# Kernel optimization log

Measured on AMD Instinct MI355X. Metric: run time of the kernel, lower is better.

## Reference

```python
import jax, jax.numpy as jnp
import numpy as np

B, T, F, H, O = 256, 1024, 128, 512, 64
BN_EPS = 1e-5


def setup_inputs() -> dict:
    key = jax.random.key(0)
    ks = jax.random.split(key, 24)
    p = lambda k, shape: 0.02 * jax.random.normal(k, shape, dtype=jnp.float32)
    inp = {
        "x": jax.random.normal(ks[0], (B, T, F), dtype=jnp.float32),
        "delta": jax.random.uniform(ks[1], (B, T, F), dtype=jnp.float32),
        "m": (jax.random.uniform(ks[2], (B, T, F)) > 0.5).astype(jnp.float32),
        "x_forward": jax.random.normal(ks[3], (B, T, F), dtype=jnp.float32),
        # packed-sequence style: descending number of active rows per timestep
        "batch_sizes": jnp.sort(jax.random.randint(ks[4], (T,), 1, B + 1))[::-1].astype(jnp.int32),
        "W_r": p(ks[5], (F, H)), "U_r": p(ks[6], (H, H)), "V_r": p(ks[7], (F, H)), "b_r": jnp.zeros((H,), jnp.float32),
        "W_z": p(ks[8], (F, H)), "U_z": p(ks[9], (H, H)), "V_z": p(ks[10], (F, H)), "b_z": jnp.zeros((H,), jnp.float32),
        "W": p(ks[11], (F, H)), "U": p(ks[12], (H, H)), "V": p(ks[13], (F, H)), "b": jnp.zeros((H,), jnp.float32),
        "W_gamma_x": p(ks[14], (F,)), "b_gamma_x": jnp.zeros((F,), jnp.float32),
        "W_gamma_h": p(ks[15], (F, H)), "b_gamma_h": jnp.zeros((H,), jnp.float32),
        "dec_W": p(ks[16], (H, O)), "dec_b": jnp.zeros((O,), jnp.float32),
        "bn_w": jnp.ones((H,), jnp.float32), "bn_b": jnp.zeros((H,), jnp.float32),
    }
    return inp


def reference(x, delta, m, x_forward, batch_sizes,
              W_r, U_r, V_r, b_r, W_z, U_z, V_z, b_z, W, U, V, b,
              W_gamma_x, b_gamma_x, W_gamma_h, b_gamma_h,
              dec_W, dec_b, bn_w, bn_b):
    # input decay gamma_x: [B,T,F]; hidden decay gamma_h: [B,T,H]
    gamma_x = jnp.exp(-jax.nn.relu(delta * W_gamma_x + b_gamma_x))
    gamma_h = jnp.exp(-jax.nn.relu(jnp.einsum("btf,fh->bth", m, W_gamma_h) + b_gamma_h))
    # impute observed (m==1) positions with decayed forward-fill (matches x[m.byte()] = x_replace[m.byte()])
    x_rep = gamma_x * x_forward + (1.0 - gamma_x) * 0.001
    x = jnp.where(m > 0.5, x_rep, x)

    # time-major for scan
    xT = jnp.transpose(x, (1, 0, 2))        # [T,B,F]
    mT = jnp.transpose(m, (1, 0, 2))        # [T,B,F]
    gT = jnp.transpose(gamma_h, (1, 0, 2))  # [T,B,H]
    row = jnp.arange(B)

    def step(h, inp):
        x_t, m_t, g_t, bs = inp
        mask = (row < bs)[:, None]          # active rows this step
        h_d = jnp.where(mask, g_t * h, h)   # decayed hidden (index_copy_ on [:bs])
        one_m = 1.0 - m_t
        z = jax.nn.sigmoid(x_t @ W_z + h_d @ U_z + one_m @ V_z + b_z)
        r = jax.nn.sigmoid(x_t @ W_r + h_d @ U_r + one_m @ V_r + b_r)
        h_tilde = jnp.tanh(x_t @ W + (h_d * r) @ U + one_m @ V + b)
        h_new = jnp.where(mask, (1.0 - z) * h_d + z * h_tilde, h_d)
        return h_new, None

    h0 = jnp.zeros((B, H), jnp.float32)
    h_t, _ = jax.lax.scan(step, h0, (xT, mT, gT, batch_sizes))

    # eval-mode BatchNorm1d (running_mean=0, running_var=1); batch_size>1 so BN applies
    h_bn = h_t * (bn_w / jnp.sqrt(1.0 + BN_EPS)) + bn_b
    output = jax.nn.log_softmax(h_bn @ dec_W + dec_b, axis=-1)
    return output, h_bn
```

## Files before the change

### kernel.cpp

```cpp
#include <hip/hip_runtime.h>
#include <hip/hip_bf16.h>

typedef __attribute__((ext_vector_type(8))) short bf16x8;
typedef __attribute__((ext_vector_type(4))) float f32x4;
typedef __attribute__((ext_vector_type(4))) float fvec4;
typedef __attribute__((ext_vector_type(4))) unsigned short u16x4;
typedef __attribute__((ext_vector_type(4))) int i32x4;

#define DEVI __device__ __forceinline__

constexpr int BB = 256, TT = 1024, FF = 128, HH = 512, OO = 64;
constexpr int KK = 256;
constexpr int NN = 2048;

DEVI unsigned short f2bf(float x) {
  unsigned int u = __float_as_uint(x);
  u += 0x7FFFu + ((u >> 16) & 1u);
  return (unsigned short)(u >> 16);
}
DEVI float bf2f(unsigned short s) {
  return __uint_as_float(((unsigned int)s) << 16);
}

DEVI void gload16(const void* g, void* lds) {
  __builtin_amdgcn_global_load_lds(
      (const __attribute__((address_space(1))) void*)g,
      (__attribute__((address_space(3))) void*)lds, 16, 0, 0);
}

DEVI void barrier_lds() {
  asm volatile("s_waitcnt lgkmcnt(0)" ::: "memory");
  __builtin_amdgcn_s_barrier();
  __builtin_amdgcn_sched_barrier(0);
}

DEVI int hgIdx(int row, int c) { return row*1024 + (c ^ ((row & 7) << 3)); }

__global__ __launch_bounds__(256) void prep_scales_kernel(
    const float* __restrict__ U_z, const float* __restrict__ U_r,
    const float* __restrict__ Uh, float* __restrict__ uscale)
{
  int n = blockIdx.x * 256 + threadIdx.x;
  if (n >= 1536) return;
  const float* src = (n < 512) ? U_z : (n < 1024) ? U_r : Uh;
  int col = n & 511;
  float s = 0.f;
  for (int k = 0; k < HH; ++k) s = fmaxf(s, fabsf(src[k*HH + col]));
  uscale[n] = fmaxf(s, 1e-30f);
}

__global__ __launch_bounds__(256) void prep_kernel(
    const float* __restrict__ W_z, const float* __restrict__ V_z, const float* __restrict__ b_z,
    const float* __restrict__ W_r, const float* __restrict__ V_r, const float* __restrict__ b_r,
    const float* __restrict__ Wh,  const float* __restrict__ Vh,  const float* __restrict__ bh,
    const float* __restrict__ Wgh, const float* __restrict__ bgh,
    const float* __restrict__ U_z, const float* __restrict__ U_r, const float* __restrict__ Uh,
    const float* __restrict__ uscale,
    unsigned short* __restrict__ BwT, float* __restrict__ bias,
    int* __restrict__ UzrQ, int* __restrict__ UhQ)
{
  int idx = blockIdx.x * 256 + threadIdx.x;
  if (idx < 524288) {
    int n = idx >> 8, k = idx & 255;
    float v;
    if (n < 512)       { int h = n;        v = (k < 128) ? W_z[k*HH + h] : -V_z[(k-128)*HH + h]; }
    else if (n < 1024) { int h = n - 512;  v = (k < 128) ? W_r[k*HH + h] : -V_r[(k-128)*HH + h]; }
    else if (n < 1536) { int h = n - 1024; v = (k < 128) ? Wh [k*HH + h] : -Vh [(k-128)*HH + h]; }
    else               { int h = n - 1536; v = (k < 128) ? 0.f : Wgh[(k-128)*HH + h]; }
    BwT[n*256 + k] = f2bf(v);
    return;
  }
  idx -= 524288;
  if (idx < 2048) {
    int n = idx; float v;
    if (n < 512)       { float s = b_z[n];      for (int f = 0; f < FF; ++f) s += V_z[f*HH + n];        v = s; }
    else if (n < 1024) { int h = n-512;  float s = b_r[h]; for (int f = 0; f < FF; ++f) s += V_r[f*HH + h]; v = s; }
    else if (n < 1536) { int h = n-1024; float s = bh[h];  for (int f = 0; f < FF; ++f) s += Vh[f*HH + h];  v = s; }
    else               { v = bgh[n-1536]; }
    bias[n] = v;
    return;
  }
  idx -= 2048;
  if (idx < 131072) {
    int j0 = (idx & 3) * 4;
    int l  = (idx >> 2) & 63;
    int nt = (idx >> 8) & 63;
    int kt = idx >> 14;
    int col = (nt & 31)*16 + (l & 15);
    const float* src = (nt < 32) ? U_z : U_r;
    float sc = 127.f / uscale[(nt < 32 ? 0 : 512) + col];
    int word = 0;
#pragma unroll
    for (int b = 0; b < 4; ++b) {
      int k = kt*64 + (l >> 4)*16 + j0 + b;
      float q = fminf(fmaxf(rintf(src[k*HH + col] * sc), -127.f), 127.f);
      word |= ((int)q & 0xFF) << (8*b);
    }
    UzrQ[idx] = word;
    return;
  }
  idx -= 131072;
  if (idx < 65536) {
    int j0 = (idx & 3) * 4;
    int l  = (idx >> 2) & 63;
    int nt = (idx >> 8) & 31;
    int kt = idx >> 13;
    int col = nt*16 + (l & 15);
    float sc = 127.f / uscale[1024 + col];
    int word = 0;
#pragma unroll
    for (int b = 0; b < 4; ++b) {
      int k = kt*64 + (l >> 4)*16 + j0 + b;
      float q = fminf(fmaxf(rintf(Uh[k*HH + col] * sc), -127.f), 127.f);
      word |= ((int)q & 0xFF) << (8*b);
    }
    UhQ[idx] = word;
  }
}

__global__ __launch_bounds__(256) void build_A_kernel(
    const float* __restrict__ x, const float* __restrict__ delta,
    const float* __restrict__ mm, const float* __restrict__ xf,
    const float* __restrict__ Wgx, const float* __restrict__ bgx,
    const int* __restrict__ bs, unsigned short* __restrict__ A,
    int t0, int TC)
{
  int blk = blockIdx.x;
  int row8 = blk * 8;
  int b0  = row8 / TC;
  int tl0 = row8 % TC;
  if (b0 >= bs[t0 + tl0]) return;
  int tid = threadIdx.x;
  int rl = row8 + (tid >> 5);
  int tc = tl0 + (tid >> 5);
  long gi = ((long)b0*TT + t0 + tc) * 32 + (tid & 31);
  int f0 = (tid & 31) * 4;
  fvec4 xv = ((const fvec4*)x)[gi];
  fvec4 dv = ((const fvec4*)delta)[gi];
  fvec4 mv = ((const fvec4*)mm)[gi];
  fvec4 fv = ((const fvec4*)xf)[gi];
  unsigned short ox[4], om[4];
#pragma unroll
  for (int j = 0; j < 4; ++j) {
    float g  = __expf(-fmaxf(dv[j]*Wgx[f0+j] + bgx[f0+j], 0.f));
    float xr = g*fv[j] + (1.f - g)*0.001f;
    float xi = (mv[j] > 0.5f) ? xr : xv[j];
    ox[j] = f2bf(xi); om[j] = f2bf(mv[j]);
  }
  *(u16x4*)(A + (long)rl*KK + f0)       = (u16x4){ox[0], ox[1], ox[2], ox[3]};
  *(u16x4*)(A + (long)rl*KK + 128 + f0) = (u16x4){om[0], om[1], om[2], om[3]};
}

__global__ __launch_bounds__(256) void gemm1_kernel(
    const unsigned short* __restrict__ A, const unsigned short* __restrict__ BwT,
    const float* __restrict__ bias, const int* __restrict__ bs,
    unsigned short* __restrict__ PRE, int t0, int TC)
{
  int blk = blockIdx.x;
  int nt = blk & 15;
  int mt = blk >> 4;
  {
    int m0 = mt * 128;
    int b_ = m0 / TC;
    int bcheck = (TC >= 128) ? bs[t0 + (m0 % TC)] : bs[t0];
    if (b_ >= bcheck) return;
  }
  int tid = threadIdx.x;
  int w = tid >> 6, l = tid & 63;
  int wm = w >> 1, wn = w & 1;
  int lr = l & 15, lg = l >> 4;
  int m_base = mt*128 + wm*64;
  int n_base = nt*128 + wn*64;
  const unsigned short* Aptr = A   + (long)(m_base + lr)*KK + lg*8;
  const unsigned short* Bptr = BwT + (long)(n_base + lr)*KK + lg*8;
  f32x4 acc[4][4];
#pragma unroll
  for (int i = 0; i < 4; ++i)
#pragma unroll
    for (int j = 0; j < 4; ++j) acc[i][j] = (f32x4){0.f, 0.f, 0.f, 0.f};

#pragma unroll
  for (int kt = 0; kt < 8; ++kt) {
    bf16x8 af[4], bfr[4];
#pragma unroll
    for (int i = 0; i < 4; ++i) af[i]  = *(const bf16x8*)(Aptr + (long)i*16*KK + kt*32);
#pragma unroll
    for (int i = 0; i < 4; ++i) bfr[i] = *(const bf16x8*)(Bptr + (long)i*16*KK + kt*32);
#pragma unroll
    for (int ms = 0; ms < 4; ++ms)
#pragma unroll
      for (int ns = 0; ns < 4; ++ns)
        acc[ms][ns] = __builtin_amdgcn_mfma_f32_16x16x32_bf16(af[ms], bfr[ns], acc[ms][ns], 0, 0, 0);
  }
#pragma unroll
  for (int ms = 0; ms < 4; ++ms) {
    int gm0 = m_base + ms*16 + lg*4;
#pragma unroll
    for (int ns = 0; ns < 4; ++ns) {
      int gn = n_base + ns*16 + lr;
      float bv = bias[gn];
      bool is_gamma = (gn >= 1536);
#pragma unroll
      for (int q = 0; q < 4; ++q) {
        float v = acc[ms][ns][q] + bv;
        if (is_gamma) v = __expf(-fmaxf(v, 0.f));
        PRE[(long)(gm0 + q)*NN + gn] = f2bf(v);
      }
    }
  }
}

__global__ __launch_bounds__(512) void scan_kernel(
    const unsigned short* __restrict__ PRE,
    const signed char* __restrict__ UzrQ,
    const signed char* __restrict__ UhQ,
    const float* __restrict__ uscale,
    const int* __restrict__ bs,
    float* __restrict__ h_st,
    float* __restrict__ sbuf,
    int t0, int TC)
{
  __shared__ __align__(16) signed char Ubuf[8][2][4096];
  __shared__ __align__(16) i32x4 hd_l[8*64];
  __shared__ __align__(16) unsigned short slabHG[16*1024];
  __shared__ float hm[16][524];
  __shared__ float wmax[8];

  const int tid = threadIdx.x;
  const int r0 = blockIdx.x * 16;
  if (t0 > 0 && bs[t0] <= r0) return;

  const int w = tid >> 6, l = tid & 63, lr = l & 15, lg = l >> 4;
  const size_t rowStr = (size_t)TC * NN;

  signed char* slot0 = &Ubuf[w][0][0];
  signed char* slot1 = &Ubuf[w][1][0];

  auto STAGEA = [&](int u) {
    const signed char* src = UzrQ + ((size_t)(((u>>1)*64 + (u&1)*32 + w*4)*64) + l)*16;
    signed char* dst = (u & 1) ? slot1 : slot0;
#pragma unroll
    for (int i = 0; i < 4; ++i) gload16(src + (size_t)i*1024, dst + i*1024);
  };
  auto STAGEB = [&](int u) {
    const signed char* src = UhQ + ((size_t)((u*32 + w*4)*64) + l)*16;
    signed char* dst = (u & 1) ? slot1 : slot0;
#pragma unroll
    for (int i = 0; i < 4; ++i) gload16(src + (size_t)i*1024, dst + i*1024);
  };
  auto STAGEHG = [&](const unsigned short* PREn) {
#pragma unroll
    for (int j = 0; j < 4; ++j) {
      int idx = w*4 + j;
      int row = idx >> 1;
      int phys = (idx & 1)*512 + l*8;
      int logi = phys ^ ((row & 7) << 3);
      const unsigned short* src = PREn + (size_t)row*rowStr + 1024 + logi;
      gload16(src, &slabHG[idx*512]);
    }
  };

  float zdq[4], rdq[4], hdq[4];
#pragma unroll
  for (int i = 0; i < 4; ++i) {
    int c = (w*4 + i)*16 + lr;
    zdq[i] = uscale[c]        * (1.f/16129.f);
    rdq[i] = uscale[512 + c]  * (1.f/16129.f);
    hdq[i] = uscale[1024 + c] * (1.f/16129.f);
  }
  if (tid < 8) wmax[tid] = (t0 == 0) ? 1e-20f : sbuf[blockIdx.x];

  if (t0 == 0) {
    for (int i = tid; i < 16*512; i += 512) hm[i>>9][i&511] = 0.f;
  } else {
    for (int i = tid; i < 16*512; i += 512)
      hm[i>>9][i&511] = h_st[(size_t)(r0 + (i>>9))*HH + (i&511)];
  }
  __builtin_amdgcn_sched_barrier(0);

  STAGEHG(PRE + (size_t)r0*TC*NN);
  STAGEA(0); STAGEA(1);

  for (int tc = 0; tc < TC; ++tc) {
    const int bsv = bs[t0 + tc];
    if (bsv <= r0) break;
    const int na = min(16, bsv - r0);
    const unsigned short* PREstep = PRE + ((size_t)r0*TC + tc)*NN;
    const unsigned short* PREnext = PREstep + NN;

    barrier_lds();
    asm volatile("s_waitcnt vmcnt(8)" ::: "memory");
    __builtin_amdgcn_sched_barrier(0);

    float s = wmax[0];
#pragma unroll
    for (int i = 1; i < 8; ++i) s = fmaxf(s, wmax[i]);
    const float qs = 127.f / s;

    unsigned short pzr[2][4][4];
#pragma unroll
    for (int i = 0; i < 4; ++i)
#pragma unroll
      for (int q = 0; q < 4; ++q) {
        int row = lg*4 + q, col = (w*4 + i)*16 + lr;
        const unsigned short* pb = PREstep + (size_t)row*rowStr + col;
        pzr[0][i][q] = pb[0];
        pzr[1][i][q] = pb[512];
      }
    __builtin_amdgcn_sched_barrier(0);

    {
      const int k0 = w*64 + lg*16;
      const bool act = lr < na;
      bf16x8 g0 = *(const bf16x8*)&slabHG[hgIdx(lr, 512 + k0)];
      bf16x8 g1 = *(const bf16x8*)&slabHG[hgIdx(lr, 512 + k0 + 8)];
      i32x4 qw;
#pragma unroll
      for (int d = 0; d < 4; ++d) {
        int word = 0;
#pragma unroll
        for (int b = 0; b < 4; ++b) {
          int j = d*4 + b;
          float h  = hm[lr][k0 + j];
          float gv = bf2f((unsigned short)(j < 8 ? g0[j] : g1[j-8]));
          float hd = act ? gv*h : h;
          float q  = fminf(fmaxf(rintf(hd*qs), -127.f), 127.f);
          word |= ((int)q & 0xFF) << (8*b);
        }
        qw[d] = word;
      }
      hd_l[w*64 + l] = qw;
    }

    float phv[4][4], ggv[4][4];
#pragma unroll
    for (int i = 0; i < 4; ++i)
#pragma unroll
      for (int q = 0; q < 4; ++q) {
        int row = lg*4 + q, col = (w*4 + i)*16 + lr;
        phv[i][q] = bf2f(slabHG[hgIdx(row, col)]);
        ggv[i][q] = bf2f(slabHG[hgIdx(row, 512 + col)]);
      }
    barrier_lds();

    i32x4 acc[8];
#pragma unroll
    for (int i = 0; i < 8; ++i) acc[i] = (i32x4){0, 0, 0, 0};
    i32x4 af;
#pragma unroll
    for (int u = 0; u < 16; ++u) {
      asm volatile("s_waitcnt vmcnt(4)" ::: "memory");
      __builtin_amdgcn_sched_barrier(0);
      const signed char* buf = (u & 1) ? slot1 : slot0;
      if (!(u & 1)) af = hd_l[(u>>1)*64 + l];
#pragma unroll
      for (int i = 0; i < 4; ++i) {
        i32x4 bfr = ((const i32x4*)buf)[i*64 + l];
        acc[(u&1)*4 + i] = __builtin_amdgcn_mfma_i32_16x16x64_i8(af, bfr, acc[(u&1)*4 + i], 0, 0, 0);
      }
      __builtin_amdgcn_sched_barrier(0);
      if (u < 14)       STAGEA(u + 2);
      else if (u == 14) STAGEB(0);
      else              STAGEB(1);
    }

    float zreg[4][4];
#pragma unroll
    for (int i = 0; i < 4; ++i)
#pragma unroll
      for (int q = 0; q < 4; ++q) {
        int row = lg*4 + q, col = (w*4 + i)*16 + lr;
        float az = bf2f(pzr[0][i][q]) + (float)acc[i][q]   * zdq[i] * s;
        float ar = bf2f(pzr[1][i][q]) + (float)acc[4+i][q] * rdq[i] * s;
        zreg[i][q] = 1.f/(1.f + __expf(-az));
        slabHG[hgIdx(row, col)] = f2bf(1.f/(1.f + __expf(-ar)));
      }
    barrier_lds();

    {
      const int k0 = w*64 + lg*16;
      bf16x8 r0v = *(const bf16x8*)&slabHG[hgIdx(lr, k0)];
      bf16x8 r1v = *(const bf16x8*)&slabHG[hgIdx(lr, k0 + 8)];
      i32x4 qw = hd_l[w*64 + l], nw;
#pragma unroll
      for (int d = 0; d < 4; ++d) {
        int word = qw[d], out = 0;
#pragma unroll
        for (int b = 0; b < 4; ++b) {
          int j = d*4 + b;
          int hq = (int)(signed char)((word >> (8*b)) & 0xFF);
          float rv = bf2f((unsigned short)(j < 8 ? r0v[j] : r1v[j-8]));
          float q = fminf(fmaxf(rintf((float)hq * rv), -127.f), 127.f);
          out |= ((int)q & 0xFF) << (8*b);
        }
        nw[d] = out;
      }
      hd_l[w*64 + l] = nw;
    }
    barrier_lds();

    i32x4 accB[4];
#pragma unroll
    for (int i = 0; i < 4; ++i) accB[i] = (i32x4){0, 0, 0, 0};
#pragma unroll
    for (int u = 0; u < 8; ++u) {
      asm volatile("s_waitcnt vmcnt(4)" ::: "memory");
      __builtin_amdgcn_sched_barrier(0);
      const signed char* buf = (u & 1) ? slot1 : slot0;
      i32x4 af2 = hd_l[u*64 + l];
#pragma unroll
      for (int i = 0; i < 4; ++i) {
        i32x4 bfr = ((const i32x4*)buf)[i*64 + l];
        accB[i] = __builtin_amdgcn_mfma_i32_16x16x64_i8(af2, bfr, accB[i], 0, 0, 0);
      }
      __builtin_amdgcn_sched_barrier(0);
      if (u < 6)       STAGEB(u + 2);
      else if (u == 6) STAGEHG(PREnext);
      else             STAGEA(0);
    }
    STAGEA(1);

    float mloc = 0.f;
#pragma unroll
    for (int i = 0; i < 4; ++i)
#pragma unroll
      for (int q = 0; q < 4; ++q) {
        int row = lg*4 + q, col = (w*4 + i)*16 + lr;
        float hval;
        if (row < na) {
          float ah = phv[i][q] + (float)accB[i][q] * hdq[i] * s;
          float e  = __expf(2.f*ah);
          float th = 1.f - 2.f/(e + 1.f);
          float hd = ggv[i][q] * hm[row][col];
          hval = hd + zreg[i][q]*(th - hd);
          hm[row][col] = hval;
        } else {
          hval = hm[row][col];
        }
        mloc = fmaxf(mloc, fabsf(hval));
      }
#pragma unroll
    for (int off = 32; off > 0; off >>= 1) mloc = fmaxf(mloc, __shfl_xor(mloc, off));
    if (l == 0) wmax[w] = fmaxf(mloc, 1e-20f);
  }

  asm volatile("s_waitcnt vmcnt(0)" ::: "memory");
  barrier_lds();
  for (int i = tid; i < 16*512; i += 512)
    h_st[(size_t)(r0 + (i>>9))*HH + (i&511)] = hm[i>>9][i&511];
  if (tid == 0) {
    float s = wmax[0];
#pragma unroll
    for (int i = 1; i < 8; ++i) s = fmaxf(s, wmax[i]);
    sbuf[blockIdx.x] = s;
  }
}

__global__ __launch_bounds__(64) void head_kernel(
    const float* __restrict__ h_state, const float* __restrict__ decW,
    const float* __restrict__ decb, const float* __restrict__ bnw,
    const float* __restrict__ bnb, float* __restrict__ out)
{
  int b = blockIdx.x, o = threadIdx.x;
  __shared__ float hbn[HH];
  const float s = rsqrtf(1.f + 1e-5f);
  for (int j = o; j < HH; j += 64)
    hbn[j] = h_state[(long)b*HH + j] * (bnw[j] * s) + bnb[j];
  __syncthreads();
  float acc = decb[o];
  for (int j = 0; j < HH; ++j) acc += hbn[j] * decW[j*OO + o];
  float mx = acc;
#pragma unroll
  for (int off = 32; off > 0; off >>= 1) mx = fmaxf(mx, __shfl_xor(mx, off));
  float ex = __expf(acc - mx);
  float sum = ex;
#pragma unroll
  for (int off = 32; off > 0; off >>= 1) sum += __shfl_xor(sum, off);
  out[(long)b*OO + o] = acc - mx - __logf(sum);
  for (int j = o; j < HH; j += 64)
    out[(long)BB*OO + (long)b*HH + j] = hbn[j];
}

extern "C" void kernel_launch(void* const* d_in, const int* in_sizes, int n_in,
                              void* d_out, int out_size, void* d_ws, size_t ws_size,
                              hipStream_t stream) {
  const float* x     = (const float*)d_in[0];
  const float* delta = (const float*)d_in[1];
  const float* mm    = (const float*)d_in[2];
  const float* xf    = (const float*)d_in[3];
  const int*   bs    = (const int*)  d_in[4];
  const float* W_r   = (const float*)d_in[5];
  const float* U_r   = (const float*)d_in[6];
  const float* V_r   = (const float*)d_in[7];
  const float* b_r   = (const float*)d_in[8];
  const float* W_z   = (const float*)d_in[9];
  const float* U_z   = (const float*)d_in[10];
  const float* V_z   = (const float*)d_in[11];
  const float* b_z   = (const float*)d_in[12];
  const float* W     = (const float*)d_in[13];
  const float* U     = (const float*)d_in[14];
  const float* V     = (const float*)d_in[15];
  const float* b     = (const float*)d_in[16];
  const float* Wgx   = (const float*)d_in[17];
  const float* bgx   = (const float*)d_in[18];
  const float* Wgh   = (const float*)d_in[19];
  const float* bgh   = (const float*)d_in[20];
  const float* decW  = (const float*)d_in[21];
  const float* decb  = (const float*)d_in[22];
  const float* bnw   = (const float*)d_in[23];
  const float* bnb   = (const float*)d_in[24];

  auto rnd = [](size_t v) { return (v + 255) & ~(size_t)255; };
  const size_t fixed_bytes = rnd((size_t)2048*256*2) + rnd(2048*4)
                           + rnd((size_t)512*1024) + rnd((size_t)256*1024)
                           + rnd(1536*4) + rnd(64)
                           + rnd((size_t)BB*HH*4);
  int TC = 0;
  const int cands[5] = {128, 64, 32, 16, 8};
  for (int i = 0; i < 5; ++i) {
    size_t need = fixed_bytes + rnd((size_t)BB*cands[i]*KK*2) + rnd((size_t)BB*cands[i]*NN*2);
    if (need <= ws_size) { TC = cands[i]; break; }
  }
  if (TC == 0) return;

  char* p = (char*)d_ws;
  auto alloc = [&](size_t bytes) { char* r = p; p += (bytes + 255) & ~(size_t)255; return r; };
  unsigned short* A_chunk = (unsigned short*)alloc((size_t)BB * TC * KK * 2);
  unsigned short* PREc    = (unsigned short*)alloc((size_t)BB * TC * NN * 2);
  unsigned short* BwT     = (unsigned short*)alloc((size_t)2048 * 256 * 2);
  float*          bias    = (float*)alloc(2048 * 4);
  int*            UzrQ    = (int*)alloc((size_t)512 * 1024);
  int*            UhQ     = (int*)alloc((size_t)256 * 1024);
  float*          uscale  = (float*)alloc(1536 * 4);
  float*          sbuf    = (float*)alloc(64);
  float*          h_st    = (float*)alloc((size_t)BB * HH * 4);

  prep_scales_kernel<<<6, 256, 0, stream>>>(U_z, U_r, U, uscale);
  prep_kernel<<<2824, 256, 0, stream>>>(W_z, V_z, b_z, W_r, V_r, b_r, W, V, b,
                                        Wgh, bgh, U_z, U_r, U, uscale,
                                        BwT, bias, UzrQ, UhQ);
  const int nch = TT / TC;
  for (int c = 0; c < nch; ++c) {
    int t0 = c * TC;
    build_A_kernel<<<BB*TC/8, 256, 0, stream>>>(x, delta, mm, xf, Wgx, bgx, bs,
                                                A_chunk, t0, TC);
    gemm1_kernel<<<(BB*TC/128)*16, 256, 0, stream>>>(A_chunk, BwT, bias, bs,
                                                     PREc, t0, TC);
    scan_kernel<<<16, 512, 0, stream>>>(PREc, (const signed char*)UzrQ,
                                        (const signed char*)UhQ, uscale, bs,
                                        h_st, sbuf, t0, TC);
  }
  head_kernel<<<256, 64, 0, stream>>>(h_st, decW, decb, bnw, bnb, (float*)d_out);
}
```

Before: 23.01 ms.

## Pin first K-slices of quantized U weights in registers and raise MFMA priority

Loads the first four A-stage and first two B-stage int8 weight slices of the recurrent U matrices into registers once before the time loop. Each step then reads them from registers instead of streaming them through LDS slots, so the global-to-LDS staging pipeline starts at later slices. MFMA sections are wrapped in s_setprio to favor matrix issue across waves. This costs 96 extra VGPRs per thread, which may lower occupancy or cause spills.

After: 23.27 ms. About the same (+1.1%).

```diff
diff --git a/kernel.cpp b/kernel.cpp
--- a/kernel.cpp
+++ b/kernel.cpp
@@ -270,16 +270,29 @@
   }
   if (tid < 8) wmax[tid] = (t0 == 0) ? 1e-20f : sbuf[blockIdx.x];
 
+  i32x4 pinA[4][4], pinB[2][4];
+#pragma unroll
+  for (int u = 0; u < 4; ++u)
+#pragma unroll
+    for (int i = 0; i < 4; ++i)
+      pinA[u][i] = ((const i32x4*)UzrQ)[((u>>1)*64 + (u&1)*32 + w*4 + i)*64 + l];
+#pragma unroll
+  for (int u = 0; u < 2; ++u)
+#pragma unroll
+    for (int i = 0; i < 4; ++i)
+      pinB[u][i] = ((const i32x4*)UhQ)[(u*32 + w*4 + i)*64 + l];
+
   if (t0 == 0) {
     for (int i = tid; i < 16*512; i += 512) hm[i>>9][i&511] = 0.f;
   } else {
     for (int i = tid; i < 16*512; i += 512)
       hm[i>>9][i&511] = h_st[(size_t)(r0 + (i>>9))*HH + (i&511)];
   }
+  asm volatile("s_waitcnt vmcnt(0)" ::: "memory");
   __builtin_amdgcn_sched_barrier(0);
 
   STAGEHG(PRE + (size_t)r0*TC*NN);
-  STAGEA(0); STAGEA(1);
+  STAGEA(4); STAGEA(5);
 
   for (int tc = 0; tc < TC; ++tc) {
     const int bsv = bs[t0 + tc];
@@ -346,22 +359,35 @@
     i32x4 acc[8];
 #pragma unroll
     for (int i = 0; i < 8; ++i) acc[i] = (i32x4){0, 0, 0, 0};
+    __builtin_amdgcn_s_setprio(1);
+#pragma unroll
+    for (int kt = 0; kt < 2; ++kt) {
+      i32x4 af = hd_l[kt*64 + l];
+#pragma unroll
+      for (int hf = 0; hf < 2; ++hf)
+#pragma unroll
+        for (int i = 0; i < 4; ++i)
+          acc[hf*4 + i] = __builtin_amdgcn_mfma_i32_16x16x64_i8(af, pinA[kt*2 + hf][i], acc[hf*4 + i], 0, 0, 0);
+    }
+    __builtin_amdgcn_s_setprio(0);
     i32x4 af;
 #pragma unroll
-    for (int u = 0; u < 16; ++u) {
+    for (int u = 4; u < 16; ++u) {
       asm volatile("s_waitcnt vmcnt(4)" ::: "memory");
       __builtin_amdgcn_sched_barrier(0);
       const signed char* buf = (u & 1) ? slot1 : slot0;
       if (!(u & 1)) af = hd_l[(u>>1)*64 + l];
+      __builtin_amdgcn_s_setprio(1);
 #pragma unroll
       for (int i = 0; i < 4; ++i) {
         i32x4 bfr = ((const i32x4*)buf)[i*64 + l];
         acc[(u&1)*4 + i] = __builtin_amdgcn_mfma_i32_16x16x64_i8(af, bfr, acc[(u&1)*4 + i], 0, 0, 0);
       }
+      __builtin_amdgcn_s_setprio(0);
       __builtin_amdgcn_sched_barrier(0);
       if (u < 14)       STAGEA(u + 2);
-      else if (u == 14) STAGEB(0);
-      else              STAGEB(1);
+      else if (u == 14) STAGEB(2);
+      else              STAGEB(3);
     }
 
     float zreg[4][4];
@@ -402,23 +428,34 @@
     i32x4 accB[4];
 #pragma unroll
     for (int i = 0; i < 4; ++i) accB[i] = (i32x4){0, 0, 0, 0};
-#pragma unroll
-    for (int u = 0; u < 8; ++u) {
+    __builtin_amdgcn_s_setprio(1);
+#pragma unroll
+    for (int u = 0; u < 2; ++u) {
+      i32x4 af2 = hd_l[u*64 + l];
+#pragma unroll
+      for (int i = 0; i < 4; ++i)
+        accB[i] = __builtin_amdgcn_mfma_i32_16x16x64_i8(af2, pinB[u][i], accB[i], 0, 0, 0);
+    }
+    __builtin_amdgcn_s_setprio(0);
+#pragma unroll
+    for (int u = 2; u < 8; ++u) {
       asm volatile("s_waitcnt vmcnt(4)" ::: "memory");
       __builtin_amdgcn_sched_barrier(0);
       const signed char* buf = (u & 1) ? slot1 : slot0;
       i32x4 af2 = hd_l[u*64 + l];
+      __builtin_amdgcn_s_setprio(1);
 #pragma unroll
       for (int i = 0; i < 4; ++i) {
         i32x4 bfr = ((const i32x4*)buf)[i*64 + l];
         accB[i] = __builtin_amdgcn_mfma_i32_16x16x64_i8(af2, bfr, accB[i], 0, 0, 0);
       }
+      __builtin_amdgcn_s_setprio(0);
       __builtin_amdgcn_sched_barrier(0);
       if (u < 6)       STAGEB(u + 2);
       else if (u == 6) STAGEHG(PREnext);
-      else             STAGEA(0);
-    }
-    STAGEA(1);
+      else             STAGEA(4);
+    }
+    STAGEA(5);
 
     float mloc = 0.f;
 #pragma unroll
```

## Quantize U_z/U_r to int4 held in registers, with offset correction via row sums

Applied to the files above, without the earlier changes.

Stores the z/r recurrent weights as packed unsigned 4-bit values, half the bytes of the former int8 form, and loads them straight into registers instead of staging them through LDS. Each nibble is unpacked to a byte for the int8 MFMA, and the +8 offset is removed by subtracting per-row sums of the quantized hidden state, gathered through a small shared array. This is meant to cut global traffic and LDS staging on the serial scan's critical path, and it adds setprio hints around the MFMAs. The trade is a much coarser weight quantization (±7 levels), which risks accuracy, plus extra unpack ALU work and register pressure.

After: 20.83 ms. 9.5% less time.

```diff
diff --git a/kernel.cpp b/kernel.cpp
--- a/kernel.cpp
+++ b/kernel.cpp
@@ -6,6 +6,7 @@
 typedef __attribute__((ext_vector_type(4))) float fvec4;
 typedef __attribute__((ext_vector_type(4))) unsigned short u16x4;
 typedef __attribute__((ext_vector_type(4))) int i32x4;
+typedef __attribute__((ext_vector_type(2))) unsigned int u32x2;
 
 #define DEVI __device__ __forceinline__
 
@@ -57,7 +58,7 @@
     const float* __restrict__ U_z, const float* __restrict__ U_r, const float* __restrict__ Uh,
     const float* __restrict__ uscale,
     unsigned short* __restrict__ BwT, float* __restrict__ bias,
-    int* __restrict__ UzrQ, int* __restrict__ UhQ)
+    unsigned int* __restrict__ UzrN, int* __restrict__ UhQ)
 {
   int idx = blockIdx.x * 256 + threadIdx.x;
   if (idx < 524288) {
@@ -81,25 +82,29 @@
     return;
   }
   idx -= 2048;
-  if (idx < 131072) {
-    int j0 = (idx & 3) * 4;
-    int l  = (idx >> 2) & 63;
-    int nt = (idx >> 8) & 63;
-    int kt = idx >> 14;
-    int col = (nt & 31)*16 + (l & 15);
-    const float* src = (nt < 32) ? U_z : U_r;
-    float sc = 127.f / uscale[(nt < 32 ? 0 : 512) + col];
-    int word = 0;
-#pragma unroll
-    for (int b = 0; b < 4; ++b) {
-      int k = kt*64 + (l >> 4)*16 + j0 + b;
-      float q = fminf(fmaxf(rintf(src[k*HH + col] * sc), -127.f), 127.f);
-      word |= ((int)q & 0xFF) << (8*b);
-    }
-    UzrQ[idx] = word;
+  if (idx < 65536) {
+    int c  = idx & 1;
+    int l  = (idx >> 1) & 63;
+    int i  = (idx >> 7) & 3;
+    int wv = (idx >> 9) & 7;
+    int u  = idx >> 12;
+    int kt = u >> 1, half = u & 1;
+    int col = (wv*4 + i)*16 + (l & 15);
+    const float* src = half ? U_r : U_z;
+    float sc = 7.f / uscale[half*512 + col];
+    unsigned int word = 0;
+#pragma unroll
+    for (int p = 0; p < 8; ++p) {
+      int j = c*8 + (p & 1)*4 + (p >> 1);
+      int k = kt*64 + (l >> 4)*16 + j;
+      float q = fminf(fmaxf(rintf(src[k*HH + col] * sc), -7.f), 7.f);
+      unsigned int uq = (unsigned int)((int)q + 8);
+      word |= (uq & 0xF) << (4*p);
+    }
+    UzrN[idx] = word;
     return;
   }
-  idx -= 131072;
+  idx -= 65536;
   if (idx < 65536) {
     int j0 = (idx & 3) * 4;
     int l  = (idx >> 2) & 63;
@@ -210,9 +215,9 @@
   }
 }
 
-__global__ __launch_bounds__(512) void scan_kernel(
+__global__ __launch_bounds__(512, 2) void scan_kernel(
     const unsigned short* __restrict__ PRE,
-    const signed char* __restrict__ UzrQ,
+    const unsigned int* __restrict__ UzrN,
     const signed char* __restrict__ UhQ,
     const float* __restrict__ uscale,
     const int* __restrict__ bs,
@@ -224,6 +229,7 @@
   __shared__ __align__(16) i32x4 hd_l[8*64];
   __shared__ __align__(16) unsigned short slabHG[16*1024];
   __shared__ float hm[16][524];
+  __shared__ int hsumW[8][16];
   __shared__ float wmax[8];
 
   const int tid = threadIdx.x;
@@ -236,12 +242,6 @@
   signed char* slot0 = &Ubuf[w][0][0];
   signed char* slot1 = &Ubuf[w][1][0];
 
-  auto STAGEA = [&](int u) {
-    const signed char* src = UzrQ + ((size_t)(((u>>1)*64 + (u&1)*32 + w*4)*64) + l)*16;
-    signed char* dst = (u & 1) ? slot1 : slot0;
-#pragma unroll
-    for (int i = 0; i < 4; ++i) gload16(src + (size_t)i*1024, dst + i*1024);
-  };
   auto STAGEB = [&](int u) {
     const signed char* src = UhQ + ((size_t)((u*32 + w*4)*64) + l)*16;
     signed char* dst = (u & 1) ? slot1 : slot0;
@@ -259,13 +259,18 @@
       gload16(src, &slabHG[idx*512]);
     }
   };
+  auto LOADZR = [&](int u, u32x2* d) {
+#pragma unroll
+    for (int i = 0; i < 4; ++i)
+      d[i] = ((const u32x2*)UzrN)[((u*8 + w)*4 + i)*64 + l];
+  };
 
   float zdq[4], rdq[4], hdq[4];
 #pragma unroll
   for (int i = 0; i < 4; ++i) {
     int c = (w*4 + i)*16 + lr;
-    zdq[i] = uscale[c]        * (1.f/16129.f);
-    rdq[i] = uscale[512 + c]  * (1.f/16129.f);
+    zdq[i] = uscale[c]        * (1.f/889.f);
+    rdq[i] = uscale[512 + c]  * (1.f/889.f);
     hdq[i] = uscale[1024 + c] * (1.f/16129.f);
   }
   if (tid < 8) wmax[tid] = (t0 == 0) ? 1e-20f : sbuf[blockIdx.x];
@@ -276,10 +281,11 @@
     for (int i = tid; i < 16*512; i += 512)
       hm[i>>9][i&511] = h_st[(size_t)(r0 + (i>>9))*HH + (i&511)];
   }
+  asm volatile("s_waitcnt vmcnt(0)" ::: "memory");
   __builtin_amdgcn_sched_barrier(0);
 
   STAGEHG(PRE + (size_t)r0*TC*NN);
-  STAGEA(0); STAGEA(1);
+  STAGEB(0); STAGEB(1);
 
   for (int tc = 0; tc < TC; ++tc) {
     const int bsv = bs[t0 + tc];
@@ -307,7 +313,10 @@
         pzr[0][i][q] = pb[0];
         pzr[1][i][q] = pb[512];
       }
-    __builtin_amdgcn_sched_barrier(0);
+
+    u32x2 inW0[4], inW1[4];
+    LOADZR(0, inW0);
+    LOADZR(1, inW1);
 
     {
       const int k0 = w*64 + lg*16;
@@ -315,6 +324,7 @@
       bf16x8 g0 = *(const bf16x8*)&slabHG[hgIdx(lr, 512 + k0)];
       bf16x8 g1 = *(const bf16x8*)&slabHG[hgIdx(lr, 512 + k0 + 8)];
       i32x4 qw;
+      int psum = 0;
 #pragma unroll
       for (int d = 0; d < 4; ++d) {
         int word = 0;
@@ -325,11 +335,16 @@
           float gv = bf2f((unsigned short)(j < 8 ? g0[j] : g1[j-8]));
           float hd = act ? gv*h : h;
           float q  = fminf(fmaxf(rintf(hd*qs), -127.f), 127.f);
-          word |= ((int)q & 0xFF) << (8*b);
+          int qi = (int)q;
+          psum += qi;
+          word |= (qi & 0xFF) << (8*b);
         }
         qw[d] = word;
       }
       hd_l[w*64 + l] = qw;
+      psum += __shfl_xor(psum, 16);
+      psum += __shfl_xor(psum, 32);
+      if (lg == 0) hsumW[w][lr] = psum;
     }
 
     float phv[4][4], ggv[4][4];
@@ -349,29 +364,39 @@
     i32x4 af;
 #pragma unroll
     for (int u = 0; u < 16; ++u) {
-      asm volatile("s_waitcnt vmcnt(4)" ::: "memory");
-      __builtin_amdgcn_sched_barrier(0);
-      const signed char* buf = (u & 1) ? slot1 : slot0;
       if (!(u & 1)) af = hd_l[(u>>1)*64 + l];
+      u32x2* inw = (u & 1) ? inW1 : inW0;
+      __builtin_amdgcn_s_setprio(1);
 #pragma unroll
       for (int i = 0; i < 4; ++i) {
-        i32x4 bfr = ((const i32x4*)buf)[i*64 + l];
+        unsigned int W0 = inw[i][0], W1 = inw[i][1];
+        i32x4 bfr;
+        bfr[0] = (int)(W0 & 0x0F0F0F0Fu);
+        bfr[1] = (int)((W0 >> 4) & 0x0F0F0F0Fu);
+        bfr[2] = (int)(W1 & 0x0F0F0F0Fu);
+        bfr[3] = (int)((W1 >> 4) & 0x0F0F0F0Fu);
         acc[(u&1)*4 + i] = __builtin_amdgcn_mfma_i32_16x16x64_i8(af, bfr, acc[(u&1)*4 + i], 0, 0, 0);
       }
-      __builtin_amdgcn_sched_barrier(0);
-      if (u < 14)       STAGEA(u + 2);
-      else if (u == 14) STAGEB(0);
-      else              STAGEB(1);
-    }
-
+      __builtin_amdgcn_s_setprio(0);
+      if (u < 14) LOADZR(u + 2, (u & 1) ? inW1 : inW0);
+    }
+
+    int rsum[4];
+#pragma unroll
+    for (int q = 0; q < 4; ++q) {
+      int row = lg*4 + q, t = 0;
+#pragma unroll
+      for (int w2 = 0; w2 < 8; ++w2) t += hsumW[w2][row];
+      rsum[q] = t * 8;
+    }
     float zreg[4][4];
 #pragma unroll
     for (int i = 0; i < 4; ++i)
 #pragma unroll
       for (int q = 0; q < 4; ++q) {
         int row = lg*4 + q, col = (w*4 + i)*16 + lr;
-        float az = bf2f(pzr[0][i][q]) + (float)acc[i][q]   * zdq[i] * s;
-        float ar = bf2f(pzr[1][i][q]) + (float)acc[4+i][q] * rdq[i] * s;
+        float az = bf2f(pzr[0][i][q]) + (float)(acc[i][q]   - rsum[q]) * zdq[i] * s;
+        float ar = bf2f(pzr[1][i][q]) + (float)(acc[4+i][q] - rsum[q]) * rdq[i] * s;
         zreg[i][q] = 1.f/(1.f + __expf(-az));
         slabHG[hgIdx(row, col)] = f2bf(1.f/(1.f + __expf(-ar)));
       }
@@ -408,17 +433,19 @@
       __builtin_amdgcn_sched_barrier(0);
       const signed char* buf = (u & 1) ? slot1 : slot0;
       i32x4 af2 = hd_l[u*64 + l];
+      __builtin_amdgcn_s_setprio(1);
 #pragma unroll
       for (int i = 0; i < 4; ++i) {
         i32x4 bfr = ((const i32x4*)buf)[i*64 + l];
         accB[i] = __builtin_amdgcn_mfma_i32_16x16x64_i8(af2, bfr, accB[i], 0, 0, 0);
       }
+      __builtin_amdgcn_s_setprio(0);
       __builtin_amdgcn_sched_barrier(0);
       if (u < 6)       STAGEB(u + 2);
       else if (u == 6) STAGEHG(PREnext);
-      else             STAGEA(0);
-    }
-    STAGEA(1);
+      else             STAGEB(0);
+    }
+    STAGEB(1);
 
     float mloc = 0.f;
 #pragma unroll
@@ -512,7 +539,7 @@
 
   auto rnd = [](size_t v) { return (v + 255) & ~(size_t)255; };
   const size_t fixed_bytes = rnd((size_t)2048*256*2) + rnd(2048*4)
-                           + rnd((size_t)512*1024) + rnd((size_t)256*1024)
+                           + rnd((size_t)256*1024) + rnd((size_t)256*1024)
                            + rnd(1536*4) + rnd(64)
                            + rnd((size_t)BB*HH*4);
   int TC = 0;
@@ -529,16 +556,16 @@
   unsigned short* PREc    = (unsigned short*)alloc((size_t)BB * TC * NN * 2);
   unsigned short* BwT     = (unsigned short*)alloc((size_t)2048 * 256 * 2);
   float*          bias    = (float*)alloc(2048 * 4);
-  int*            UzrQ    = (int*)alloc((size_t)512 * 1024);
+  unsigned int*   UzrN    = (unsigned int*)alloc((size_t)256 * 1024);
   int*            UhQ     = (int*)alloc((size_t)256 * 1024);
   float*          uscale  = (float*)alloc(1536 * 4);
   float*          sbuf    = (float*)alloc(64);
   float*          h_st    = (float*)alloc((size_t)BB * HH * 4);
 
   prep_scales_kernel<<<6, 256, 0, stream>>>(U_z, U_r, U, uscale);
-  prep_kernel<<<2824, 256, 0, stream>>>(W_z, V_z, b_z, W_r, V_r, b_r, W, V, b,
+  prep_kernel<<<2568, 256, 0, stream>>>(W_z, V_z, b_z, W_r, V_r, b_r, W, V, b,
                                         Wgh, bgh, U_z, U_r, U, uscale,
-                                        BwT, bias, UzrQ, UhQ);
+                                        BwT, bias, UzrN, UhQ);
   const int nch = TT / TC;
   for (int c = 0; c < nch; ++c) {
     int t0 = c * TC;
@@ -546,9 +573,8 @@
                                                 A_chunk, t0, TC);
     gemm1_kernel<<<(BB*TC/128)*16, 256, 0, stream>>>(A_chunk, BwT, bias, bs,
                                                      PREc, t0, TC);
-    scan_kernel<<<16, 512, 0, stream>>>(PREc, (const signed char*)UzrQ,
-                                        (const signed char*)UhQ, uscale, bs,
-                                        h_st, sbuf, t0, TC);
+    scan_kernel<<<16, 512, 0, stream>>>(PREc, UzrN, (const signed char*)UhQ,
+                                        uscale, bs, h_st, sbuf, t0, TC);
   }
   head_kernel<<<256, 64, 0, stream>>>(h_st, decW, decb, bnw, bnb, (float*)d_out);
 }
```
